# Kernel tuning notes

Measured on AMD Instinct MI355X. Metric: run time of the kernel, lower is better.

The kernel has to match this reference:

```python
import jax, jax.numpy as jnp
import numpy as np

N = 50000      # nodes
E = 500000     # edges
IN = 256       # input feature dim
HID = 64       # hidden (per-head) dim, layer 1
H1 = 4         # heads, layer 1
NC = 64        # num_classes (layer 2 out, 1 head)
ED = 32        # edge_dim
T = 8          # num_etypes
SLOPE = 0.2    # leakyrelu negative slope


def setup_inputs() -> dict:
    key = jax.random.key(0)
    ks = jax.random.split(key, 20)
    p = lambda k, shape: (jax.random.normal(k, shape, jnp.float32) * 0.05)
    return {
        "h": jax.random.normal(ks[0], (N, IN), jnp.float32),
        "row": jax.random.randint(ks[1], (E,), 0, N, jnp.int32),   # src
        "col": jax.random.randint(ks[2], (E,), 0, N, jnp.int32),   # dst
        "etype": jax.random.randint(ks[3], (E,), 0, T, jnp.int32),
        # layer 1 (4 heads, no residual, elu activation)
        "edge_emb1": p(ks[4], (T, ED)),
        "W1": p(ks[5], (IN, HID * H1)),
        "Wr1": p(ks[6], (T, ED, ED * H1)),      # TypedLinear per-etype weight
        "a_l1": p(ks[7], (H1, HID)),
        "a_r1": p(ks[8], (H1, HID)),
        "a_e1": p(ks[9], (H1, ED)),
        # layer 2 (1 head, residual Linear, no activation)
        "edge_emb2": p(ks[10], (T, ED)),
        "W2": p(ks[11], (HID * H1, NC)),
        "Wr2": p(ks[12], (T, ED, ED)),
        "a_l2": p(ks[13], (1, NC)),
        "a_r2": p(ks[14], (1, NC)),
        "a_e2": p(ks[15], (1, ED)),
        "res_W2": p(ks[16], (HID * H1, NC)),
        "res_b2": p(ks[17], (NC,)),
    }


def _simple_hgn_conv(h, row, col, etype, edge_emb, W, Wr, a_l, a_r, a_e,
                     res_W, res_b, apply_act):
    """One SimpleHGNConv layer. h:[N,in], returns [N, out_dim*H] (D-major, H-minor
    layout, matching emb.permute(0,2,1).view in the torch code)."""
    H, D = a_l.shape            # num_heads, out_dim
    n = h.shape[0]
    emb = (h @ W).reshape(n, H, D)                     # [N,H,D]
    emb = jnp.where(jnp.isnan(emb), 0.0, emb)
    # TypedLinear: edge_emb[etype] @ Wr[etype]; only T distinct rows -> per-type GEMM
    ee = jnp.einsum('te,teo->to', edge_emb, Wr).reshape(T, H, ED)  # [T,H,ED]
    h_l = jnp.einsum('nhd,hd->nh', emb, a_l)[row]      # [E,H]
    h_r = jnp.einsum('nhd,hd->nh', emb, a_r)[col]      # [E,H]
    h_e = jnp.einsum('thd,hd->th', ee, a_e)[etype]     # [E,H]
    att = jax.nn.leaky_relu(h_l + h_r + h_e, SLOPE)    # [E,H]
    # edge_softmax: normalize over incoming edges of each destination node (col)
    seg_max = jax.ops.segment_max(att, col, num_segments=n)   # [N,H]
    att = jnp.exp(att - seg_max[col])
    seg_sum = jax.ops.segment_sum(att, col, num_segments=n)   # [N,H]
    alpha = att / seg_sum[col]                          # [E,H]
    # u_mul_e + sum aggregation
    msg = emb[row] * alpha[:, :, None]                  # [E,H,D]
    out = jax.ops.segment_sum(msg, col, num_segments=n) # [N,H,D]
    out = out.transpose(0, 2, 1).reshape(n, D * H)      # D-major layout
    if res_W is not None:
        out = out + h @ res_W + res_b
    if apply_act:
        out = jax.nn.elu(out)
    return out


def reference(h, row, col, etype,
              edge_emb1, W1, Wr1, a_l1, a_r1, a_e1,
              edge_emb2, W2, Wr2, a_l2, a_r2, a_e2, res_W2, res_b2):
    h1 = _simple_hgn_conv(h, row, col, etype, edge_emb1, W1, Wr1,
                          a_l1, a_r1, a_e1, None, None, True)
    h2 = _simple_hgn_conv(h1, row, col, etype, edge_emb2, W2, Wr2,
                          a_l2, a_r2, a_e2, res_W2, res_b2, False)
    # split by node type (first half type 'l', second half type 'v')
    return (h2[: N // 2], h2[N // 2 :])
```

## Files before the change

kernel.cpp:

```cpp
#include <hip/hip_runtime.h>
#include <hip/hip_bf16.h>

typedef __bf16 bf16x8 __attribute__((ext_vector_type(8)));
typedef float f32x4 __attribute__((ext_vector_type(4)));

#define IN_DIM 256
#define NT 8

__device__ __forceinline__ float b2f(unsigned short u) {
  union { unsigned int i; float f; } x; x.i = ((unsigned int)u) << 16; return x.f;
}
__device__ __forceinline__ float lo2f(unsigned int w) {
  union { unsigned int i; float f; } x; x.i = w << 16; return x.f;
}
__device__ __forceinline__ float hi2f(unsigned int w) {
  union { unsigned int i; float f; } x; x.i = w & 0xFFFF0000u; return x.f;
}
__device__ __forceinline__ unsigned short f2b(float f) {
  union { float f; unsigned int i; } u; u.f = f;
  unsigned int r = u.i + 0x7FFF + ((u.i >> 16) & 1);
  return (unsigned short)(r >> 16);
}
__device__ __forceinline__ float lrelu(float x) { return x >= 0.f ? x : 0.2f * x; }
__device__ __forceinline__ float ldf(const void* p, size_t i, int isf32) {
  return isf32 ? ((const float*)p)[i] : b2f(((const unsigned short*)p)[i]);
}

__global__ void prep_all_kernel(const void* __restrict__ W1, const void* __restrict__ W2,
                                const void* __restrict__ rW2,
                                const void* __restrict__ al1, const void* __restrict__ ar1,
                                const void* __restrict__ al2, const void* __restrict__ ar2,
                                const void* __restrict__ ee1, const void* __restrict__ Wr1,
                                const void* __restrict__ ae1,
                                const void* __restrict__ ee2, const void* __restrict__ Wr2,
                                const void* __restrict__ ae2,
                                unsigned short* __restrict__ W1t,
                                unsigned short* __restrict__ W2t,
                                float* __restrict__ a2l, float* __restrict__ a2r,
                                float* __restrict__ he1, float* __restrict__ he2,
                                float* __restrict__ alD, float* __restrict__ arD,
                                const unsigned int* __restrict__ hw,
                                const int* __restrict__ col, int* __restrict__ cnt,
                                int E_, int N_, int* __restrict__ dflag) {
  int b = blockIdx.x, tid = threadIdx.x;
  if (b >= 454) {
    int base = (b - 454) * 1024 + tid;
#pragma unroll
    for (int k = 0; k < 4; k++) {
      int e = base + k * 256;
      if (e < E_) {
        int c = col[e];
        if ((unsigned)c < (unsigned)N_) atomicAdd(&cnt[c], 1);
      }
    }
    return;
  }
  __shared__ int sflag;
  {
    int bad = 0;
    if (tid < 64) {
      for (int i = 0; i < 4; i++) {
        unsigned int w = hw[tid * 4 + i];
        unsigned int ex = (w & 0x7FFFu) >> 7;
        if (ex >= 0xC0u) bad++;
      }
#pragma unroll
      for (int off = 32; off; off >>= 1) bad += __shfl_xor(bad, off);
      if (tid == 0) sflag = (bad > 8) ? 1 : 0;
    }
    __syncthreads();
  }
  const int isf32 = sflag;
  if (b == 0 && tid == 0) *dflag = isf32;
  if (b < 384) {
    int j = b, k = tid;
    if (j < 256) {
      int src = (j & 3) * 64 + (j >> 2);
      W1t[j * 256 + k] = f2b(ldf(W1, (size_t)k * 256 + src, isf32));
    } else {
      int o = j - 256;
      float v = (o < 64) ? ldf(W2, (size_t)k * 64 + o, isf32)
                         : ldf(rW2, (size_t)k * 64 + (o - 64), isf32);
      W2t[o * 256 + k] = f2b(v);
    }
  } else if (b < 448) {
    int k = (b - 384) * 4 + (tid >> 6), d = tid & 63;
    float w2 = ldf(W2, (size_t)k * 64 + d, isf32);
    float l2 = w2 * ldf(al2, d, isf32);
    float r2 = w2 * ldf(ar2, d, isf32);
#pragma unroll
    for (int off = 32; off; off >>= 1) { l2 += __shfl_xor(l2, off); r2 += __shfl_xor(r2, off); }
    if (d == 0) { a2l[k] = l2; a2r[k] = r2; }
  } else {
    int bid = b - 448;
    int t = tid >> 5, d = tid & 31;
    if (bid < 4) {
      int h = bid;
      float s = 0.f;
#pragma unroll
      for (int e = 0; e < 32; e++)
        s += ldf(ee1, t * 32 + e, isf32) * ldf(Wr1, (size_t)(t * 32 + e) * 128 + h * 32 + d, isf32);
      float v = s * ldf(ae1, h * 32 + d, isf32);
#pragma unroll
      for (int off = 16; off; off >>= 1) v += __shfl_xor(v, off);
      if (d == 0) he1[t * 4 + h] = v;
    } else if (bid == 4) {
      float s = 0.f;
#pragma unroll
      for (int e = 0; e < 32; e++)
        s += ldf(ee2, t * 32 + e, isf32) * ldf(Wr2, (size_t)(t * 32 + e) * 32 + d, isf32);
      float v = s * ldf(ae2, d, isf32);
#pragma unroll
      for (int off = 16; off; off >>= 1) v += __shfl_xor(v, off);
      if (d == 0) he2[t] = v;
    } else {
      int j = tid;
      alD[j] = ldf(al1, (j & 3) * 64 + (j >> 2), isf32);
      arD[j] = ldf(ar1, (j & 3) * 64 + (j >> 2), isf32);
    }
  }
}

__global__ __launch_bounds__(256, 2) void gemm1_fill(
    const void* __restrict__ A, int M,
    const unsigned short* __restrict__ Bt,
    unsigned short* __restrict__ emb1,
    const float* __restrict__ alD, const float* __restrict__ arD,
    float* __restrict__ hl1, float* __restrict__ hr1,
    const int* __restrict__ dflag, int MBlocks,
    const int* __restrict__ col, const int* __restrict__ row,
    const int* __restrict__ ety, const int* __restrict__ ptrb,
    const int* __restrict__ bsum, int* __restrict__ cnt,
    int* __restrict__ srcc, int E_) {
  __shared__ unsigned short As[64 * 64];
  __shared__ unsigned short Bs[256 * 64];
  __shared__ float lsum[4][64][4];
  __shared__ float rsum[4][64][4];
  if (blockIdx.x >= MBlocks) {
    int base = (blockIdx.x - MBlocks) * 1024 + threadIdx.x;
#pragma unroll
    for (int k = 0; k < 4; k++) {
      int e = base + k * 256;
      if (e < E_) {
        int c = col[e];
        if ((unsigned)c < (unsigned)M) {
          int pos = atomicSub(&cnt[c], 1) - 1;
          long long slot = (long long)(ptrb[c] + bsum[c >> 8]) + pos;
          if (slot >= 0 && slot < E_) {
            int sr = row[e], t = ety[e];
            srcc[slot] = ((unsigned)sr < (unsigned)M && (unsigned)t < (unsigned)NT)
                             ? (sr | (t << 20)) : -1;
          }
        }
      }
    }
    return;
  }
  int isf32 = *dflag;
  const int tid = threadIdx.x;
  const int m0 = blockIdx.x * 64;
  const int wv = tid >> 6, lane = tid & 63;
  const int q = lane >> 4, m = lane & 15;
  const int jp = wv * 64;
  f32x4 acc[4][4] = {};
  for (int kc = 0; kc < 256; kc += 64) {
    {
      int row_ = tid >> 2, qt = tid & 3;
      int gr = m0 + row_;
      unsigned short tmp[16];
      if (gr < M) {
        if (isf32) {
          const float* ap = (const float*)A + (size_t)gr * 256 + kc + qt * 16;
          float4 v0 = *(const float4*)ap;
          float4 v1 = *(const float4*)(ap + 4);
          float4 v2 = *(const float4*)(ap + 8);
          float4 v3 = *(const float4*)(ap + 12);
          tmp[0]=f2b(v0.x); tmp[1]=f2b(v0.y); tmp[2]=f2b(v0.z); tmp[3]=f2b(v0.w);
          tmp[4]=f2b(v1.x); tmp[5]=f2b(v1.y); tmp[6]=f2b(v1.z); tmp[7]=f2b(v1.w);
          tmp[8]=f2b(v2.x); tmp[9]=f2b(v2.y); tmp[10]=f2b(v2.z); tmp[11]=f2b(v2.w);
          tmp[12]=f2b(v3.x); tmp[13]=f2b(v3.y); tmp[14]=f2b(v3.z); tmp[15]=f2b(v3.w);
        } else {
          const unsigned short* ap = (const unsigned short*)A + (size_t)gr * 256 + kc + qt * 16;
          *(int4*)tmp = *(const int4*)ap;
          *(int4*)(tmp + 8) = *(const int4*)(ap + 8);
        }
      } else {
        for (int x = 0; x < 16; x++) tmp[x] = 0;
      }
      int g0 = (qt * 2) ^ (row_ & 7);
      int g1 = (qt * 2 + 1) ^ (row_ & 7);
      *(int4*)(As + row_ * 64 + g0 * 8) = *(int4*)tmp;
      *(int4*)(As + row_ * 64 + g1 * 8) = *(int4*)(tmp + 8);
    }
    {
#pragma unroll
      for (int i = 0; i < 8; i++) {
        int id = tid + i * 256;
        int row_ = id >> 3, gg = id & 7;
        int4 v = *(const int4*)(Bt + (size_t)row_ * 256 + kc + gg * 8);
        int pg = gg ^ (row_ & 7);
        *(int4*)(Bs + row_ * 64 + pg * 8) = v;
      }
    }
    __syncthreads();
#pragma unroll
    for (int ks = 0; ks < 2; ks++) {
      int gk = ks * 4 + q;
      bf16x8 afr[4];
#pragma unroll
      for (int cm = 0; cm < 4; cm++) {
        int row_ = cm * 16 + m;
        afr[cm] = *(const bf16x8*)(As + row_ * 64 + (gk ^ (row_ & 7)) * 8);
      }
#pragma unroll
      for (int cj = 0; cj < 4; cj++) {
        int jr = jp + cj * 16 + m;
        bf16x8 b = *(const bf16x8*)(Bs + jr * 64 + (gk ^ (jr & 7)) * 8);
#pragma unroll
        for (int cm = 0; cm < 4; cm++)
          acc[cm][cj] = __builtin_amdgcn_mfma_f32_16x16x32_bf16(afr[cm], b, acc[cm][cj], 0, 0, 0);
      }
    }
    __syncthreads();
  }
  float al[4], ar[4];
#pragma unroll
  for (int cj = 0; cj < 4; cj++) {
    al[cj] = alD[jp + cj * 16 + m];
    ar[cj] = arD[jp + cj * 16 + m];
  }
#pragma unroll
  for (int cm = 0; cm < 4; cm++) {
#pragma unroll
    for (int r = 0; r < 4; r++) {
      int lrow = cm * 16 + q * 4 + r;
      int gm = m0 + lrow;
      float lp = 0.f, rp = 0.f;
#pragma unroll
      for (int cj = 0; cj < 4; cj++) {
        float v = acc[cm][cj][r];
        if (gm < M) emb1[(size_t)gm * 256 + jp + cj * 16 + m] = f2b(v);
        lp += v * al[cj]; rp += v * ar[cj];
      }
      lp += __shfl_xor(lp, 4); lp += __shfl_xor(lp, 8);
      rp += __shfl_xor(rp, 4); rp += __shfl_xor(rp, 8);
      if (m < 4) { lsum[wv][lrow][m] = lp; rsum[wv][lrow][m] = rp; }
    }
  }
  __syncthreads();
  {
    int row_ = tid >> 2, h = tid & 3;
    int gm = m0 + row_;
    if (gm < M) {
      float l = lsum[0][row_][h] + lsum[1][row_][h] + lsum[2][row_][h] + lsum[3][row_][h];
      float r = rsum[0][row_][h] + rsum[1][row_][h] + rsum[2][row_][h] + rsum[3][row_][h];
      hl1[(size_t)gm * 4 + h] = l;
      hr1[(size_t)gm * 4 + h] = r;
    }
  }
}

__global__ __launch_bounds__(256, 2) void gemm2_fused(
    const unsigned short* __restrict__ A, int M,
    const unsigned short* __restrict__ Bt,
    unsigned short* __restrict__ emb2, unsigned short* __restrict__ res,
    const void* __restrict__ bias, const int* __restrict__ dflag) {
  __shared__ unsigned short As[64 * 64];
  __shared__ unsigned short Bs[128 * 64];
  int isf32 = *dflag;
  const int tid = threadIdx.x;
  const int m0 = blockIdx.x * 64;
  const int wv = tid >> 6, lane = tid & 63;
  const int q = lane >> 4, m = lane & 15;
  const int jp = (wv & 1) * 64;
  const int mh = (wv >> 1) * 32;
  f32x4 acc[2][4] = {};
  for (int kc = 0; kc < 256; kc += 64) {
    {
      int row = tid >> 2, qt = tid & 3;
      int gr = m0 + row;
      unsigned short tmp[16];
      if (gr < M) {
        const unsigned short* ap = A + (size_t)gr * 256 + kc + qt * 16;
        *(int4*)tmp = *(const int4*)ap;
        *(int4*)(tmp + 8) = *(const int4*)(ap + 8);
      } else {
        for (int x = 0; x < 16; x++) tmp[x] = 0;
      }
      int g0 = (qt * 2) ^ (row & 7);
      int g1 = (qt * 2 + 1) ^ (row & 7);
      *(int4*)(As + row * 64 + g0 * 8) = *(int4*)tmp;
      *(int4*)(As + row * 64 + g1 * 8) = *(int4*)(tmp + 8);
    }
    {
#pragma unroll
      for (int i = 0; i < 4; i++) {
        int id = tid + i * 256;
        int row = id >> 3, gg = id & 7;
        int4 v = *(const int4*)(Bt + (size_t)row * 256 + kc + gg * 8);
        int pg = gg ^ (row & 7);
        *(int4*)(Bs + row * 64 + pg * 8) = v;
      }
    }
    __syncthreads();
#pragma unroll
    for (int ks = 0; ks < 2; ks++) {
      int gk = ks * 4 + q;
      bf16x8 afr[2];
#pragma unroll
      for (int cm = 0; cm < 2; cm++) {
        int row = mh + cm * 16 + m;
        afr[cm] = *(const bf16x8*)(As + row * 64 + (gk ^ (row & 7)) * 8);
      }
#pragma unroll
      for (int cj = 0; cj < 4; cj++) {
        int jr = jp + cj * 16 + m;
        bf16x8 b = *(const bf16x8*)(Bs + jr * 64 + (gk ^ (jr & 7)) * 8);
#pragma unroll
        for (int cm = 0; cm < 2; cm++)
          acc[cm][cj] = __builtin_amdgcn_mfma_f32_16x16x32_bf16(afr[cm], b, acc[cm][cj], 0, 0, 0);
      }
    }
    __syncthreads();
  }
  float bv[4];
#pragma unroll
  for (int cj = 0; cj < 4; cj++)
    bv[cj] = (jp == 64) ? ldf(bias, cj * 16 + m, isf32) : 0.f;
#pragma unroll
  for (int cm = 0; cm < 2; cm++) {
#pragma unroll
    for (int r = 0; r < 4; r++) {
      int gm = m0 + mh + cm * 16 + q * 4 + r;
      if (gm < M) {
#pragma unroll
        for (int cj = 0; cj < 4; cj++) {
          float v = acc[cm][cj][r];
          int gj = cj * 16 + m;
          if (jp == 0) emb2[(size_t)gm * 64 + gj] = f2b(v);
          else res[(size_t)gm * 64 + gj] = f2b(v + bv[cj]);
        }
      }
    }
  }
}

__global__ void scan1_kernel(const int* __restrict__ cnt, int* __restrict__ ptrb,
                             int* __restrict__ bsum, int n) {
  __shared__ int wsum[4];
  int tid = threadIdx.x, lane = tid & 63, wid = tid >> 6;
  int i = blockIdx.x * 256 + tid;
  int v = (i < n) ? cnt[i] : 0;
  int x = v;
#pragma unroll
  for (int off = 1; off < 64; off <<= 1) {
    int y = __shfl_up(x, off);
    if (lane >= off) x += y;
  }
  if (lane == 63) wsum[wid] = x;
  __syncthreads();
  int woff = 0;
#pragma unroll
  for (int k = 0; k < 4; k++) woff += (k < wid) ? wsum[k] : 0;
  if (i < n) ptrb[i] = x - v + woff;
  if (tid == 255) bsum[blockIdx.x] = woff + x;
}

__global__ void scan2_kernel(int* __restrict__ bsum, int* __restrict__ ptrb,
                             int nb, int n) {
  __shared__ int wsum[4];
  int tid = threadIdx.x, lane = tid & 63, wid = tid >> 6;
  int v = (tid < nb) ? bsum[tid] : 0;
  int x = v;
#pragma unroll
  for (int off = 1; off < 64; off <<= 1) {
    int y = __shfl_up(x, off);
    if (lane >= off) x += y;
  }
  if (lane == 63) wsum[wid] = x;
  __syncthreads();
  int woff = 0;
#pragma unroll
  for (int k = 0; k < 4; k++) woff += (k < wid) ? wsum[k] : 0;
  if (tid < nb) bsum[tid] = x - v + woff;
  if (tid == 255) ptrb[n] = woff + x;
}

__global__ __launch_bounds__(256) void agg1_kernel(
    const int* __restrict__ ptrb, const int* __restrict__ bsumv,
    const int* __restrict__ srcc,
    const float* __restrict__ hl1, const float* __restrict__ hr1,
    const float* __restrict__ he1,
    const unsigned short* __restrict__ emb1, unsigned short* __restrict__ h1,
    const float* __restrict__ a2l, const float* __restrict__ a2r,
    float* __restrict__ hl2, float* __restrict__ hr2,
    int n0, int N_, int E_) {
  __shared__ float4 wds[4][64];
  __shared__ int sds[4][64];
  const int tid = threadIdx.x;
  const int wv = tid >> 6, lane = tid & 63;
  const int g = lane >> 4, ln = lane & 15;
  const int node = n0 + blockIdx.x * 16 + wv * 4 + g;
  const bool nv = node < N_;
  int p0 = 0, p1 = 0;
  if (nv) {
    p0 = ptrb[node] + bsumv[node >> 8];
    p1 = (node + 1 < N_) ? (ptrb[node + 1] + bsumv[(node + 1) >> 8]) : ptrb[N_];
    p0 = max(0, min(p0, E_)); p1 = max(p0, min(p1, E_));
  }
  float4 hrv = {0.f, 0.f, 0.f, 0.f};
  if (nv) hrv = *(const float4*)(hr1 + 4 * (size_t)node);
  float s0 = 0.f, s1 = 0.f, s2 = 0.f, s3 = 0.f;
  float acc[16];
#pragma unroll
  for (int k = 0; k < 16; k++) acc[k] = 0.f;
  const unsigned short* erow = emb1 + ln * 16;
  for (int pb = p0;; pb += 16) {
    if (!__any(pb < p1)) break;
    int mc = (pb < p1) ? min(p1 - pb, 16) : 0;
    float4 w = {0.f, 0.f, 0.f, 0.f};
    int src = 0;
    if (ln < mc) {
      int spk = srcc[pb + ln];
      if (spk >= 0) {
        int sr = spk & 0xFFFFF, t = spk >> 20;
        float4 a = *(const float4*)(hl1 + 4 * (size_t)sr);
        float4 ge = *(const float4*)(he1 + 4 * (size_t)t);
        w.x = __expf(lrelu(a.x + hrv.x + ge.x));
        w.y = __expf(lrelu(a.y + hrv.y + ge.y));
        w.z = __expf(lrelu(a.z + hrv.z + ge.z));
        w.w = __expf(lrelu(a.w + hrv.w + ge.w));
        src = sr;
      }
    }
    s0 += w.x; s1 += w.y; s2 += w.z; s3 += w.w;
    wds[wv][lane] = w;
    sds[wv][lane] = src;
    for (int j = 0; j < mc; j += 2) {
      bool v1 = (j + 1) < mc;
      float4 u0 = wds[wv][g * 16 + j];
      int r0 = sds[wv][g * 16 + j];
      const unsigned short* e0 = erow + (size_t)r0 * 256;
      int4 ra = *(const int4*)e0;
      int4 rb = *(const int4*)(e0 + 8);
      float4 u1; int4 rc, rd;
      if (v1) {
        u1 = wds[wv][g * 16 + j + 1];
        int r1 = sds[wv][g * 16 + j + 1];
        const unsigned short* e1 = erow + (size_t)r1 * 256;
        rc = *(const int4*)e1;
        rd = *(const int4*)(e1 + 8);
      }
      acc[0]  += u0.x * lo2f(ra.x); acc[1]  += u0.y * hi2f(ra.x);
      acc[2]  += u0.z * lo2f(ra.y); acc[3]  += u0.w * hi2f(ra.y);
      acc[4]  += u0.x * lo2f(ra.z); acc[5]  += u0.y * hi2f(ra.z);
      acc[6]  += u0.z * lo2f(ra.w); acc[7]  += u0.w * hi2f(ra.w);
      acc[8]  += u0.x * lo2f(rb.x); acc[9]  += u0.y * hi2f(rb.x);
      acc[10] += u0.z * lo2f(rb.y); acc[11] += u0.w * hi2f(rb.y);
      acc[12] += u0.x * lo2f(rb.z); acc[13] += u0.y * hi2f(rb.z);
      acc[14] += u0.z * lo2f(rb.w); acc[15] += u0.w * hi2f(rb.w);
      if (v1) {
        acc[0]  += u1.x * lo2f(rc.x); acc[1]  += u1.y * hi2f(rc.x);
        acc[2]  += u1.z * lo2f(rc.y); acc[3]  += u1.w * hi2f(rc.y);
        acc[4]  += u1.x * lo2f(rc.z); acc[5]  += u1.y * hi2f(rc.z);
        acc[6]  += u1.z * lo2f(rc.w); acc[7]  += u1.w * hi2f(rc.w);
        acc[8]  += u1.x * lo2f(rd.x); acc[9]  += u1.y * hi2f(rd.x);
        acc[10] += u1.z * lo2f(rd.y); acc[11] += u1.w * hi2f(rd.y);
        acc[12] += u1.x * lo2f(rd.z); acc[13] += u1.y * hi2f(rd.z);
        acc[14] += u1.z * lo2f(rd.w); acc[15] += u1.w * hi2f(rd.w);
      }
    }
  }
#pragma unroll
  for (int off = 1; off < 16; off <<= 1) {
    s0 += __shfl_xor(s0, off); s1 += __shfl_xor(s1, off);
    s2 += __shfl_xor(s2, off); s3 += __shfl_xor(s3, off);
  }
  float invs[4];
  invs[0] = s0 > 0.f ? 1.f / s0 : 0.f;
  invs[1] = s1 > 0.f ? 1.f / s1 : 0.f;
  invs[2] = s2 > 0.f ? 1.f / s2 : 0.f;
  invs[3] = s3 > 0.f ? 1.f / s3 : 0.f;
  float alv[16], arv[16];
#pragma unroll
  for (int q2 = 0; q2 < 4; q2++) {
    float4 t1 = *(const float4*)(a2l + ln * 16 + q2 * 4);
    float4 t2 = *(const float4*)(a2r + ln * 16 + q2 * 4);
    alv[q2 * 4 + 0] = t1.x; alv[q2 * 4 + 1] = t1.y;
    alv[q2 * 4 + 2] = t1.z; alv[q2 * 4 + 3] = t1.w;
    arv[q2 * 4 + 0] = t2.x; arv[q2 * 4 + 1] = t2.y;
    arv[q2 * 4 + 2] = t2.z; arv[q2 * 4 + 3] = t2.w;
  }
  float lp = 0.f, rp = 0.f;
  unsigned int ow[8];
#pragma unroll
  for (int k = 0; k < 16; k++) {
    float r = acc[k] * invs[k & 3];
    r = r > 0.f ? r : __expf(r) - 1.f;
    unsigned int bb = f2b(r);
    if ((k & 1) == 0) ow[k >> 1] = bb; else ow[k >> 1] |= bb << 16;
    lp += r * alv[k];
    rp += r * arv[k];
  }
  if (nv) {
    int4 va; va.x = ow[0]; va.y = ow[1]; va.z = ow[2]; va.w = ow[3];
    int4 vb; vb.x = ow[4]; vb.y = ow[5]; vb.z = ow[6]; vb.w = ow[7];
    *(int4*)(h1 + (size_t)node * 256 + ln * 16) = va;
    *(int4*)(h1 + (size_t)node * 256 + ln * 16 + 8) = vb;
  }
#pragma unroll
  for (int off = 1; off < 16; off <<= 1) {
    lp += __shfl_xor(lp, off); rp += __shfl_xor(rp, off);
  }
  if (nv && ln == 0) { hl2[node] = lp; hr2[node] = rp; }
}

__global__ __launch_bounds__(256) void agg2_kernel(
    const int* __restrict__ ptrb, const int* __restrict__ bsumv,
    const int* __restrict__ srcc,
    const float* __restrict__ hl2, const float* __restrict__ hr2,
    const float* __restrict__ he2,
    const unsigned short* __restrict__ emb2, const unsigned short* __restrict__ res,
    void* __restrict__ out, int N_, int E_, const int* __restrict__ dflag) {
  __shared__ int2 wsd[4][4][17];
  const int isf32 = *dflag;
  const int tid = threadIdx.x;
  const int wv = tid >> 6, lane = tid & 63;
  const int g = lane >> 4, ln = lane & 15;
  const int node = blockIdx.x * 16 + wv * 4 + g;
  const bool nv = node < N_;
  int p0 = 0, p1 = 0;
  if (nv) {
    p0 = ptrb[node] + bsumv[node >> 8];
    p1 = (node + 1 < N_) ? (ptrb[node + 1] + bsumv[(node + 1) >> 8]) : ptrb[N_];
    p0 = max(0, min(p0, E_)); p1 = max(p0, min(p1, E_));
  }
  float hrv = nv ? hr2[node] : 0.f;
  float s = 0.f;
  float acc[4] = {0.f, 0.f, 0.f, 0.f};
  const unsigned short* erow = emb2 + ln * 4;
  for (int pb = p0;; pb += 16) {
    if (!__any(pb < p1)) break;
    int mc = (pb < p1) ? min(p1 - pb, 16) : 0;
    float w = 0.f; int src = 0;
    if (ln < mc) {
      int spk = srcc[pb + ln];
      if (spk >= 0) {
        int sr = spk & 0xFFFFF, t = spk >> 20;
        w = __expf(lrelu(hl2[sr] + hrv + he2[t]));
        src = sr;
      }
    }
    s += w;
    int2 pk; pk.x = __float_as_int(w); pk.y = src;
    wsd[wv][g][ln] = pk;
    int2 w0 = {0, 0}, w1 = {0, 0}; int2 pa = {0, 0}, pc = {0, 0};
    if (0 < mc) { w0 = wsd[wv][g][0]; pa = *(const int2*)(erow + (size_t)w0.y * 64); }
    if (1 < mc) { w1 = wsd[wv][g][1]; pc = *(const int2*)(erow + (size_t)w1.y * 64); }
    for (int j = 0; j < mc; j += 2) {
      int2 nw0 = {0, 0}, nw1 = {0, 0}, na = {0, 0}, nc = {0, 0};
      if (j + 2 < mc) { nw0 = wsd[wv][g][j + 2]; na = *(const int2*)(erow + (size_t)nw0.y * 64); }
      if (j + 3 < mc) { nw1 = wsd[wv][g][j + 3]; nc = *(const int2*)(erow + (size_t)nw1.y * 64); }
      float u0 = __int_as_float(w0.x);
      acc[0] += u0 * lo2f(pa.x); acc[1] += u0 * hi2f(pa.x);
      acc[2] += u0 * lo2f(pa.y); acc[3] += u0 * hi2f(pa.y);
      if (j + 1 < mc) {
        float u1 = __int_as_float(w1.x);
        acc[0] += u1 * lo2f(pc.x); acc[1] += u1 * hi2f(pc.x);
        acc[2] += u1 * lo2f(pc.y); acc[3] += u1 * hi2f(pc.y);
      }
      w0 = nw0; w1 = nw1; pa = na; pc = nc;
    }
  }
#pragma unroll
  for (int off = 1; off < 16; off <<= 1) s += __shfl_xor(s, off);
  float inv = s > 0.f ? 1.f / s : 0.f;
  if (nv) {
    ushort4 rv = *(const ushort4*)(res + (size_t)node * 64 + ln * 4);
    float o0 = acc[0] * inv + b2f(rv.x);
    float o1 = acc[1] * inv + b2f(rv.y);
    float o2 = acc[2] * inv + b2f(rv.z);
    float o3 = acc[3] * inv + b2f(rv.w);
    size_t oi = (size_t)node * 64 + ln * 4;
    if (isf32) {
      float4 ov = {o0, o1, o2, o3};
      *(float4*)((float*)out + oi) = ov;
    } else {
      ushort4 ov; ov.x = f2b(o0); ov.y = f2b(o1); ov.z = f2b(o2); ov.w = f2b(o3);
      *(ushort4*)((unsigned short*)out + oi) = ov;
    }
  }
}

extern "C" void kernel_launch(void* const* d_in, const int* in_sizes, int n_in,
                              void* d_out, int out_size, void* d_ws, size_t ws_size,
                              hipStream_t stream) {
  const int N = in_sizes[0] / IN_DIM;
  const int E = in_sizes[1];

  const void* h   = d_in[0];
  const int* row  = (const int*)d_in[1];
  const int* col  = (const int*)d_in[2];
  const int* ety  = (const int*)d_in[3];
  const void* ee1 = d_in[4];
  const void* W1  = d_in[5];
  const void* Wr1 = d_in[6];
  const void* al1 = d_in[7];
  const void* ar1 = d_in[8];
  const void* ae1 = d_in[9];
  const void* ee2 = d_in[10];
  const void* W2  = d_in[11];
  const void* Wr2 = d_in[12];
  const void* al2 = d_in[13];
  const void* ar2 = d_in[14];
  const void* ae2 = d_in[15];
  const void* rW2 = d_in[16];
  const void* rb2 = d_in[17];

  char* p = (char*)d_ws;
  auto take = [&](size_t b) { char* q = p; p += (b + 255) & ~(size_t)255; return q; };
  unsigned short* h1   = (unsigned short*)take((size_t)N * 256 * 2);
  unsigned short* emb1 = (unsigned short*)take((size_t)N * 256 * 2);
  int* srcc = (int*)take((size_t)E * 4);
  int* ptrb = (int*)take((size_t)(N + 1) * 4);
  int* cnt  = (int*)take((size_t)N * 4);
  int* bsum = (int*)take(1024);
  float* hl1 = (float*)take((size_t)N * 4 * 4);
  float* hr1 = (float*)take((size_t)N * 4 * 4);
  float* hl2 = (float*)take((size_t)N * 4);
  float* hr2 = (float*)take((size_t)N * 4);
  unsigned short* W1t = (unsigned short*)take(256 * 256 * 2);
  unsigned short* W2t = (unsigned short*)take(128 * 256 * 2);
  float* a2l = (float*)take(256 * 4);
  float* a2r = (float*)take(256 * 4);
  float* alD = (float*)take(256 * 4);
  float* arD = (float*)take(256 * 4);
  float* he1 = (float*)take(NT * 4 * 4);
  float* he2 = (float*)take(NT * 4);
  int* dflag = (int*)take(256);
  unsigned short* emb2 = emb1;
  unsigned short* res  = emb1 + (size_t)N * 64;

  const size_t need = (size_t)(p - (char*)d_ws);
  if (need > ws_size) {
    hipMemsetAsync(d_out, 0, (size_t)out_size * 2, stream);
    return;
  }

  const int ECB = (E + 1023) / 1024;
  const int MB = (N + 63) / 64;
  const int SB = (N + 255) / 256;
  const int AB = (N + 15) / 16;

  hipMemsetAsync(cnt, 0, (size_t)N * 4, stream);
  prep_all_kernel<<<454 + ECB, 256, 0, stream>>>(
      W1, W2, rW2, al1, ar1, al2, ar2, ee1, Wr1, ae1, ee2, Wr2, ae2,
      W1t, W2t, a2l, a2r, he1, he2, alD, arD,
      (const unsigned int*)h, col, cnt, E, N, dflag);

  scan1_kernel<<<SB, 256, 0, stream>>>(cnt, ptrb, bsum, N);
  scan2_kernel<<<1, 256, 0, stream>>>(bsum, ptrb, SB, N);

  gemm1_fill<<<MB + ECB, 256, 0, stream>>>(
      h, N, W1t, emb1, alD, arD, hl1, hr1, dflag, MB,
      col, row, ety, ptrb, bsum, cnt, srcc, E);

  const int ABh = AB / 2;
  if (ABh > 0)
    agg1_kernel<<<ABh, 256, 0, stream>>>(
        ptrb, bsum, srcc, hl1, hr1, he1, emb1, h1, a2l, a2r, hl2, hr2, 0, N, E);
  agg1_kernel<<<AB - ABh, 256, 0, stream>>>(
      ptrb, bsum, srcc, hl1, hr1, he1, emb1, h1, a2l, a2r, hl2, hr2, ABh * 16, N, E);

  gemm2_fused<<<MB, 256, 0, stream>>>(h1, N, W2t, emb2, res, rb2, dflag);
  agg2_kernel<<<AB, 256, 0, stream>>>(
      ptrb, bsum, srcc, hl2, hr2, he2, emb2, res, d_out, N, E, dflag);
}
```

Baseline: 265.0 us.

## Read GEMM B fragments directly from global memory and raise occupancy

In both GEMM kernels the shared-memory staging of the weight tile B is removed. MFMA B fragments are now loaded straight from global or L2, since the weights are small and shared by every block. The LDS savings allow launch bounds of 4 blocks per CU instead of 2, for more occupancy and latency hiding. The two split agg1 launches are also merged into one, removing a launch. The risk is global-load latency inside the MFMA inner loop and possibly more register pressure under the tighter launch bound.

```diff
diff --git a/kernel.cpp b/kernel.cpp
--- a/kernel.cpp
+++ b/kernel.cpp
@@ -121,7 +121,7 @@
   }
 }
 
-__global__ __launch_bounds__(256, 2) void gemm1_fill(
+__global__ __launch_bounds__(256, 4) void gemm1_fill(
     const void* __restrict__ A, int M,
     const unsigned short* __restrict__ Bt,
     unsigned short* __restrict__ emb1,
@@ -133,7 +133,6 @@
     const int* __restrict__ bsum, int* __restrict__ cnt,
     int* __restrict__ srcc, int E_) {
   __shared__ unsigned short As[64 * 64];
-  __shared__ unsigned short Bs[256 * 64];
   __shared__ float lsum[4][64][4];
   __shared__ float rsum[4][64][4];
   if (blockIdx.x >= MBlocks) {
@@ -192,16 +191,6 @@
       *(int4*)(As + row_ * 64 + g0 * 8) = *(int4*)tmp;
       *(int4*)(As + row_ * 64 + g1 * 8) = *(int4*)(tmp + 8);
     }
-    {
-#pragma unroll
-      for (int i = 0; i < 8; i++) {
-        int id = tid + i * 256;
-        int row_ = id >> 3, gg = id & 7;
-        int4 v = *(const int4*)(Bt + (size_t)row_ * 256 + kc + gg * 8);
-        int pg = gg ^ (row_ & 7);
-        *(int4*)(Bs + row_ * 64 + pg * 8) = v;
-      }
-    }
     __syncthreads();
 #pragma unroll
     for (int ks = 0; ks < 2; ks++) {
@@ -215,7 +204,7 @@
 #pragma unroll
       for (int cj = 0; cj < 4; cj++) {
         int jr = jp + cj * 16 + m;
-        bf16x8 b = *(const bf16x8*)(Bs + jr * 64 + (gk ^ (jr & 7)) * 8);
+        bf16x8 b = *(const bf16x8*)(Bt + (size_t)jr * 256 + kc + gk * 8);
 #pragma unroll
         for (int cm = 0; cm < 4; cm++)
           acc[cm][cj] = __builtin_amdgcn_mfma_f32_16x16x32_bf16(afr[cm], b, acc[cm][cj], 0, 0, 0);
@@ -260,13 +249,12 @@
   }
 }
 
-__global__ __launch_bounds__(256, 2) void gemm2_fused(
+__global__ __launch_bounds__(256, 4) void gemm2_fused(
     const unsigned short* __restrict__ A, int M,
     const unsigned short* __restrict__ Bt,
     unsigned short* __restrict__ emb2, unsigned short* __restrict__ res,
     const void* __restrict__ bias, const int* __restrict__ dflag) {
   __shared__ unsigned short As[64 * 64];
-  __shared__ unsigned short Bs[128 * 64];
   int isf32 = *dflag;
   const int tid = threadIdx.x;
   const int m0 = blockIdx.x * 64;
@@ -292,16 +280,6 @@
       *(int4*)(As + row * 64 + g0 * 8) = *(int4*)tmp;
       *(int4*)(As + row * 64 + g1 * 8) = *(int4*)(tmp + 8);
     }
-    {
-#pragma unroll
-      for (int i = 0; i < 4; i++) {
-        int id = tid + i * 256;
-        int row = id >> 3, gg = id & 7;
-        int4 v = *(const int4*)(Bt + (size_t)row * 256 + kc + gg * 8);
-        int pg = gg ^ (row & 7);
-        *(int4*)(Bs + row * 64 + pg * 8) = v;
-      }
-    }
     __syncthreads();
 #pragma unroll
     for (int ks = 0; ks < 2; ks++) {
@@ -315,7 +293,7 @@
 #pragma unroll
       for (int cj = 0; cj < 4; cj++) {
         int jr = jp + cj * 16 + m;
-        bf16x8 b = *(const bf16x8*)(Bs + jr * 64 + (gk ^ (jr & 7)) * 8);
+        bf16x8 b = *(const bf16x8*)(Bt + (size_t)jr * 256 + kc + gk * 8);
 #pragma unroll
         for (int cm = 0; cm < 2; cm++)
           acc[cm][cj] = __builtin_amdgcn_mfma_f32_16x16x32_bf16(afr[cm], b, acc[cm][cj], 0, 0, 0);
@@ -665,12 +643,8 @@
       h, N, W1t, emb1, alD, arD, hl1, hr1, dflag, MB,
       col, row, ety, ptrb, bsum, cnt, srcc, E);
 
-  const int ABh = AB / 2;
-  if (ABh > 0)
-    agg1_kernel<<<ABh, 256, 0, stream>>>(
-        ptrb, bsum, srcc, hl1, hr1, he1, emb1, h1, a2l, a2r, hl2, hr2, 0, N, E);
-  agg1_kernel<<<AB - ABh, 256, 0, stream>>>(
-      ptrb, bsum, srcc, hl1, hr1, he1, emb1, h1, a2l, a2r, hl2, hr2, ABh * 16, N, E);
+  agg1_kernel<<<AB, 256, 0, stream>>>(
+      ptrb, bsum, srcc, hl1, hr1, he1, emb1, h1, a2l, a2r, hl2, hr2, 0, N, E);
 
   gemm2_fused<<<MB, 256, 0, stream>>>(h1, N, W2t, emb2, res, rb2, dflag);
   agg2_kernel<<<AB, 256, 0, stream>>>(
```

Measured after the change: 269.3 us. About the same (+1.6%).

## Register-prefetch next K tile in GEMMs, reorder fill blocks, merge agg1 launches

Applied to the files above, without the earlier changes.

Both GEMM kernels now load the next 64-wide K slice of A and B into registers right after the barrier, so global loads overlap the MFMA work on the current slice. In gemm1_fill the edge-fill blocks move to the front of the grid so the scatter work is scheduled first. The two split agg1 launches are merged into one launch. The prefetch costs extra registers per thread, which may reduce occupancy under the launch bounds.

```diff
diff --git a/kernel.cpp b/kernel.cpp
--- a/kernel.cpp
+++ b/kernel.cpp
@@ -127,7 +127,7 @@
     unsigned short* __restrict__ emb1,
     const float* __restrict__ alD, const float* __restrict__ arD,
     float* __restrict__ hl1, float* __restrict__ hr1,
-    const int* __restrict__ dflag, int MBlocks,
+    const int* __restrict__ dflag, int FillBlocks,
     const int* __restrict__ col, const int* __restrict__ row,
     const int* __restrict__ ety, const int* __restrict__ ptrb,
     const int* __restrict__ bsum, int* __restrict__ cnt,
@@ -136,8 +136,8 @@
   __shared__ unsigned short Bs[256 * 64];
   __shared__ float lsum[4][64][4];
   __shared__ float rsum[4][64][4];
-  if (blockIdx.x >= MBlocks) {
-    int base = (blockIdx.x - MBlocks) * 1024 + threadIdx.x;
+  if (blockIdx.x < FillBlocks) {
+    int base = blockIdx.x * 1024 + threadIdx.x;
 #pragma unroll
     for (int k = 0; k < 4; k++) {
       int e = base + k * 256;
@@ -158,51 +158,67 @@
   }
   int isf32 = *dflag;
   const int tid = threadIdx.x;
-  const int m0 = blockIdx.x * 64;
+  const int m0 = (blockIdx.x - FillBlocks) * 64;
   const int wv = tid >> 6, lane = tid & 63;
   const int q = lane >> 4, m = lane & 15;
   const int jp = wv * 64;
+  const int arow = tid >> 2, aqt = tid & 3;
+  const int gr = m0 + arow;
   f32x4 acc[4][4] = {};
+  int4 aR[4];
+  int4 bR[8];
+  aR[0] = aR[1] = aR[2] = aR[3] = (int4){0, 0, 0, 0};
+
+  auto loadA = [&](int kc) {
+    if (gr < M) {
+      if (isf32) {
+        const float* ap = (const float*)A + (size_t)gr * 256 + kc + aqt * 16;
+        aR[0] = *(const int4*)ap;
+        aR[1] = *(const int4*)(ap + 4);
+        aR[2] = *(const int4*)(ap + 8);
+        aR[3] = *(const int4*)(ap + 12);
+      } else {
+        const unsigned short* ap = (const unsigned short*)A + (size_t)gr * 256 + kc + aqt * 16;
+        aR[0] = *(const int4*)ap;
+        aR[1] = *(const int4*)(ap + 8);
+      }
+    }
+  };
+  auto loadB = [&](int kc) {
+#pragma unroll
+    for (int i = 0; i < 8; i++) {
+      int id = tid + i * 256;
+      int brow = id >> 3, bg = id & 7;
+      bR[i] = *(const int4*)(Bt + (size_t)brow * 256 + kc + bg * 8);
+    }
+  };
+
+  loadA(0); loadB(0);
   for (int kc = 0; kc < 256; kc += 64) {
     {
-      int row_ = tid >> 2, qt = tid & 3;
-      int gr = m0 + row_;
       unsigned short tmp[16];
-      if (gr < M) {
-        if (isf32) {
-          const float* ap = (const float*)A + (size_t)gr * 256 + kc + qt * 16;
-          float4 v0 = *(const float4*)ap;
-          float4 v1 = *(const float4*)(ap + 4);
-          float4 v2 = *(const float4*)(ap + 8);
-          float4 v3 = *(const float4*)(ap + 12);
-          tmp[0]=f2b(v0.x); tmp[1]=f2b(v0.y); tmp[2]=f2b(v0.z); tmp[3]=f2b(v0.w);
-          tmp[4]=f2b(v1.x); tmp[5]=f2b(v1.y); tmp[6]=f2b(v1.z); tmp[7]=f2b(v1.w);
-          tmp[8]=f2b(v2.x); tmp[9]=f2b(v2.y); tmp[10]=f2b(v2.z); tmp[11]=f2b(v2.w);
-          tmp[12]=f2b(v3.x); tmp[13]=f2b(v3.y); tmp[14]=f2b(v3.z); tmp[15]=f2b(v3.w);
-        } else {
-          const unsigned short* ap = (const unsigned short*)A + (size_t)gr * 256 + kc + qt * 16;
-          *(int4*)tmp = *(const int4*)ap;
-          *(int4*)(tmp + 8) = *(const int4*)(ap + 8);
-        }
+      if (isf32) {
+        const float* f = (const float*)aR;
+#pragma unroll
+        for (int x = 0; x < 16; x++) tmp[x] = f2b(f[x]);
       } else {
-        for (int x = 0; x < 16; x++) tmp[x] = 0;
-      }
-      int g0 = (qt * 2) ^ (row_ & 7);
-      int g1 = (qt * 2 + 1) ^ (row_ & 7);
-      *(int4*)(As + row_ * 64 + g0 * 8) = *(int4*)tmp;
-      *(int4*)(As + row_ * 64 + g1 * 8) = *(int4*)(tmp + 8);
-    }
-    {
+        *(int4*)tmp = aR[0];
+        *(int4*)(tmp + 8) = aR[1];
+      }
+      int g0 = (aqt * 2) ^ (arow & 7);
+      int g1 = (aqt * 2 + 1) ^ (arow & 7);
+      *(int4*)(As + arow * 64 + g0 * 8) = *(int4*)tmp;
+      *(int4*)(As + arow * 64 + g1 * 8) = *(int4*)(tmp + 8);
 #pragma unroll
       for (int i = 0; i < 8; i++) {
         int id = tid + i * 256;
-        int row_ = id >> 3, gg = id & 7;
-        int4 v = *(const int4*)(Bt + (size_t)row_ * 256 + kc + gg * 8);
-        int pg = gg ^ (row_ & 7);
-        *(int4*)(Bs + row_ * 64 + pg * 8) = v;
+        int brow = id >> 3, bg = id & 7;
+        int pg = bg ^ (brow & 7);
+        *(int4*)(Bs + brow * 64 + pg * 8) = bR[i];
       }
     }
     __syncthreads();
+    if (kc < 192) { loadA(kc + 64); loadB(kc + 64); }
 #pragma unroll
     for (int ks = 0; ks < 2; ks++) {
       int gk = ks * 4 + q;
@@ -274,35 +290,44 @@
   const int q = lane >> 4, m = lane & 15;
   const int jp = (wv & 1) * 64;
   const int mh = (wv >> 1) * 32;
+  const int arow = tid >> 2, aqt = tid & 3;
+  const int gr = m0 + arow;
   f32x4 acc[2][4] = {};
+  int4 aR[2];
+  int4 bR[4];
+  aR[0] = aR[1] = (int4){0, 0, 0, 0};
+  auto loadA = [&](int kc) {
+    if (gr < M) {
+      const unsigned short* ap = A + (size_t)gr * 256 + kc + aqt * 16;
+      aR[0] = *(const int4*)ap;
+      aR[1] = *(const int4*)(ap + 8);
+    }
+  };
+  auto loadB = [&](int kc) {
+#pragma unroll
+    for (int i = 0; i < 4; i++) {
+      int id = tid + i * 256;
+      int brow = id >> 3, bg = id & 7;
+      bR[i] = *(const int4*)(Bt + (size_t)brow * 256 + kc + bg * 8);
+    }
+  };
+  loadA(0); loadB(0);
   for (int kc = 0; kc < 256; kc += 64) {
     {
-      int row = tid >> 2, qt = tid & 3;
-      int gr = m0 + row;
-      unsigned short tmp[16];
-      if (gr < M) {
-        const unsigned short* ap = A + (size_t)gr * 256 + kc + qt * 16;
-        *(int4*)tmp = *(const int4*)ap;
-        *(int4*)(tmp + 8) = *(const int4*)(ap + 8);
-      } else {
-        for (int x = 0; x < 16; x++) tmp[x] = 0;
-      }
-      int g0 = (qt * 2) ^ (row & 7);
-      int g1 = (qt * 2 + 1) ^ (row & 7);
-      *(int4*)(As + row * 64 + g0 * 8) = *(int4*)tmp;
-      *(int4*)(As + row * 64 + g1 * 8) = *(int4*)(tmp + 8);
-    }
-    {
+      int g0 = (aqt * 2) ^ (arow & 7);
+      int g1 = (aqt * 2 + 1) ^ (arow & 7);
+      *(int4*)(As + arow * 64 + g0 * 8) = aR[0];
+      *(int4*)(As + arow * 64 + g1 * 8) = aR[1];
 #pragma unroll
       for (int i = 0; i < 4; i++) {
         int id = tid + i * 256;
-        int row = id >> 3, gg = id & 7;
-        int4 v = *(const int4*)(Bt + (size_t)row * 256 + kc + gg * 8);
-        int pg = gg ^ (row & 7);
-        *(int4*)(Bs + row * 64 + pg * 8) = v;
+        int brow = id >> 3, bg = id & 7;
+        int pg = bg ^ (brow & 7);
+        *(int4*)(Bs + brow * 64 + pg * 8) = bR[i];
       }
     }
     __syncthreads();
+    if (kc < 192) { loadA(kc + 64); loadB(kc + 64); }
 #pragma unroll
     for (int ks = 0; ks < 2; ks++) {
       int gk = ks * 4 + q;
@@ -661,16 +686,12 @@
   scan1_kernel<<<SB, 256, 0, stream>>>(cnt, ptrb, bsum, N);
   scan2_kernel<<<1, 256, 0, stream>>>(bsum, ptrb, SB, N);
 
-  gemm1_fill<<<MB + ECB, 256, 0, stream>>>(
-      h, N, W1t, emb1, alD, arD, hl1, hr1, dflag, MB,
+  gemm1_fill<<<ECB + MB, 256, 0, stream>>>(
+      h, N, W1t, emb1, alD, arD, hl1, hr1, dflag, ECB,
       col, row, ety, ptrb, bsum, cnt, srcc, E);
 
-  const int ABh = AB / 2;
-  if (ABh > 0)
-    agg1_kernel<<<ABh, 256, 0, stream>>>(
-        ptrb, bsum, srcc, hl1, hr1, he1, emb1, h1, a2l, a2r, hl2, hr2, 0, N, E);
-  agg1_kernel<<<AB - ABh, 256, 0, stream>>>(
-      ptrb, bsum, srcc, hl1, hr1, he1, emb1, h1, a2l, a2r, hl2, hr2, ABh * 16, N, E);
+  agg1_kernel<<<AB, 256, 0, stream>>>(
+      ptrb, bsum, srcc, hl1, hr1, he1, emb1, h1, a2l, a2r, hl2, hr2, 0, N, E);
 
   gemm2_fused<<<MB, 256, 0, stream>>>(h1, N, W2t, emb2, res, rb2, dflag);
   agg2_kernel<<<AB, 256, 0, stream>>>(
```

Measured after the change: 325.1 us. 1.23x slower.
